# Kernel optimization log

Measured on AMD Instinct MI355X. Metric: run time of the kernel, lower is better.

The kernel has to match this reference:

```python
import jax, jax.numpy as jnp
import numpy as np

B, T_SRC, T_TGT = 2048, 32, 32
D = 512            # d_model
D_SRC, D_TGT = 100, 80
L = 2              # n_layers


def setup_inputs() -> dict:
    key = jax.random.key(0)
    ks = jax.random.split(key, 16)
    s = 1.0 / float(np.sqrt(D))  # torch LSTM init scale
    u = lambda k, shape: jax.random.uniform(k, shape, jnp.float32, -s, s)
    return {
        "src": jax.random.randint(ks[0], (B, T_SRC), 0, D_SRC, dtype=jnp.int32),
        "tgt": jax.random.randint(ks[1], (B, T_TGT), 0, D_TGT, dtype=jnp.int32),
        "enc_emb": jax.random.normal(ks[2], (D_SRC, D), jnp.float32),
        "dec_emb": jax.random.normal(ks[3], (D_TGT, D), jnp.float32),
        "enc_Wih": u(ks[4], (L, 4 * D, D)),
        "enc_Whh": u(ks[5], (L, 4 * D, D)),
        "enc_bih": u(ks[6], (L, 4 * D)),
        "enc_bhh": u(ks[7], (L, 4 * D)),
        "dec_Wih": u(ks[8], (L, 4 * D, D)),
        "dec_Whh": u(ks[9], (L, 4 * D, D)),
        "dec_bih": u(ks[10], (L, 4 * D)),
        "dec_bhh": u(ks[11], (L, 4 * D)),
        "post_W": u(ks[12], (D_TGT, D)),
        "post_b": u(ks[13], (D_TGT,)),
    }


def lstm_cell(x, h, c, Wih, Whh, bih, bhh):
    # PyTorch gate order: i, f, g, o
    gates = x @ Wih.T + bih + h @ Whh.T + bhh  # [B, 4D]
    i, f, g, o = jnp.split(gates, 4, axis=-1)
    c_new = jax.nn.sigmoid(f) * c + jax.nn.sigmoid(i) * jnp.tanh(g)
    h_new = jax.nn.sigmoid(o) * jnp.tanh(c_new)
    return h_new, c_new


def reference(src, tgt, enc_emb, dec_emb, enc_Wih, enc_Whh, enc_bih, enc_bhh,
              dec_Wih, dec_Whh, dec_bih, dec_bhh, post_W, post_b):
    # Eval-mode forward: dropout = identity, teacher forcing disabled
    # (tf = random() < ratio AND self.training is False at inference).
    n_layers = enc_Wih.shape[0]
    Bb = src.shape[0]
    Dm = enc_emb.shape[1]

    # ---- encoder: multi-layer LSTM over src embeddings ----
    x = enc_emb[src].swapaxes(0, 1)  # [T_src, B, D]
    hs, cs = [], []
    z = jnp.zeros((Bb, Dm), x.dtype)
    for l in range(n_layers):
        def step(carry, xt, l=l):
            h, c = carry
            h, c = lstm_cell(xt, h, c, enc_Wih[l], enc_Whh[l], enc_bih[l], enc_bhh[l])
            return (h, c), h
        (hT, cT), x = jax.lax.scan(step, (z, z), x)
        hs.append(hT)
        cs.append(cT)
    h0 = jnp.stack(hs)  # [L, B, D]
    c0 = jnp.stack(cs)  # [L, B, D]

    prev0 = dec_emb[tgt[:, 0]]  # [B, D]

    def dec_step(carry, _):
        h, c, prev = carry
        x = prev
        new_h, new_c = [], []
        for l in range(n_layers):
            hl, cl = lstm_cell(x, h[l], c[l], dec_Wih[l], dec_Whh[l], dec_bih[l], dec_bhh[l])
            new_h.append(hl)
            new_c.append(cl)
            x = hl
        logits = x @ post_W.T + post_b          # [B, d_tgt]
        pred = jnp.argmax(logits, axis=-1)       # [B]
        prev = dec_emb[pred]                     # [B, D]
        return (jnp.stack(new_h), jnp.stack(new_c), prev), logits

    _, out = jax.lax.scan(dec_step, (h0, c0, prev0), None, length=tgt.shape[1])
    return out.swapaxes(0, 1)  # [B, T_tgt, d_tgt]
```

## Files before the change

kernel.cpp:

```cpp
#include <hip/hip_runtime.h>
#include <hip/hip_bf16.h>

#define B_  2048
#define T_  32
#define D_  512
#define G_  2048
#define VT_ 80
#define BD  (B_ * D_)
#define LWE ((size_t)G_ * D_)

typedef _Float16 half8 __attribute__((ext_vector_type(8)));
typedef _Float16 half4_t __attribute__((ext_vector_type(4)));
typedef float    f32x4 __attribute__((ext_vector_type(4)));

static __device__ __forceinline__ float sigm(float x) {
    return 1.0f / (1.0f + expf(-x));
}

typedef __attribute__((address_space(1))) unsigned int gas_u32;
typedef __attribute__((address_space(3))) unsigned int las_u32;
static __device__ __forceinline__ void glds16(const void* src, void* dst) {
    __builtin_amdgcn_global_load_lds(
        (gas_u32*)(unsigned long long)(size_t)src,
        (las_u32*)(unsigned int)(size_t)dst, 16, 0, 0);
}

#define WBX() do {                                        \
    asm volatile("s_waitcnt vmcnt(10)" ::: "memory");     \
    __builtin_amdgcn_s_barrier();                         \
    __builtin_amdgcn_sched_barrier(0);                    \
} while (0)

__global__ void zero_ws(int4* __restrict__ p, int n) {
    int i = blockIdx.x * blockDim.x + threadIdx.x;
    if (i < n) p[i] = int4{0, 0, 0, 0};
}
__global__ void init_pred(const int* __restrict__ tgt, int* __restrict__ pred) {
    int i = blockIdx.x * blockDim.x + threadIdx.x;
    if (i < B_) pred[i] = tgt[i * T_];
}

__global__ void split_weights(const float* __restrict__ s0, const float* __restrict__ s1,
                              const float* __restrict__ s2, const float* __restrict__ s3,
                              const float* __restrict__ s4, const float* __restrict__ s5,
                              _Float16* __restrict__ Wbase) {
    int g = blockIdx.x * blockDim.x + threadIdx.x;
    int mat = g >> 17;
    int rem = g & 131071;
    int np  = rem >> 6;
    int kq  = rem & 63;
    const float* src = (mat == 0) ? s0 : (mat == 1) ? s1 : (mat == 2) ? s2
                     : (mat == 3) ? s3 : (mat == 4) ? s4 : s5;
    int n = (np & 3) * D_ + (np >> 2);
    const float* sp = src + (size_t)n * D_ + kq * 8;
    float4 v0 = ((const float4*)sp)[0], v1 = ((const float4*)sp)[1];
    float x[8] = {v0.x, v0.y, v0.z, v0.w, v1.x, v1.y, v1.z, v1.w};
    _Float16 hi[8], lo[8];
    #pragma unroll
    for (int u = 0; u < 8; ++u) {
        hi[u] = (_Float16)x[u];
        lo[u] = (_Float16)(x[u] - (float)hi[u]);
    }
    int tile = (np >> 4) * 16 + (kq >> 2);
    int lane = (np & 15) | ((kq & 3) << 4);
    size_t e = (size_t)tile * 512 + (size_t)lane * 8;
    _Float16* Whi = Wbase + (size_t)mat * (2 * LWE);
    _Float16* Wlo = Whi + LWE;
    *(half8*)(Whi + e) = *(half8*)hi;
    *(half8*)(Wlo + e) = *(half8*)lo;
}

__global__ void split_postW(const float* __restrict__ pw,
                            _Float16* __restrict__ Ph, _Float16* __restrict__ Pl) {
    int g = blockIdx.x * blockDim.x + threadIdx.x;
    if (g >= VT_ * 64) return;
    int v = g >> 6, kq = g & 63;
    const float* sp = pw + (size_t)v * D_ + kq * 8;
    float4 v0 = ((const float4*)sp)[0], v1 = ((const float4*)sp)[1];
    float x[8] = {v0.x, v0.y, v0.z, v0.w, v1.x, v1.y, v1.z, v1.w};
    _Float16 hi[8], lo[8];
    #pragma unroll
    for (int u = 0; u < 8; ++u) {
        hi[u] = (_Float16)x[u];
        lo[u] = (_Float16)(x[u] - (float)hi[u]);
    }
    int tile = (v >> 4) * 16 + (kq >> 2);
    int lane = (v & 15) | ((kq & 3) << 4);
    size_t e = (size_t)tile * 512 + (size_t)lane * 8;
    *(half8*)(Ph + e) = *(half8*)hi;
    *(half8*)(Pl + e) = *(half8*)lo;
}

__global__ void perm_bias(const float* __restrict__ ebih, const float* __restrict__ ebhh,
                          const float* __restrict__ dbih, const float* __restrict__ dbhh,
                          float* __restrict__ biasP) {
    int i = blockIdx.x * blockDim.x + threadIdx.x;
    int cfg = i >> 11, np = i & 2047;
    int n = (np & 3) * D_ + (np >> 2);
    const float* bi = ((cfg < 2) ? ebih : dbih) + (cfg & 1) * G_;
    const float* bh = ((cfg < 2) ? ebhh : dbhh) + (cfg & 1) * G_;
    biasP[cfg * G_ + np] = bi[n] + bh[n];
}

__global__ __launch_bounds__(256) void compute_P(
    const float* __restrict__ enc_emb, const float* __restrict__ dec_emb,
    const float* __restrict__ encW0,   const float* __restrict__ decW0,
    float* __restrict__ P) {
    __shared__ float es[10][D_];
    __shared__ float part[4][64][10];
    int by = blockIdx.y;
    bool enc = (by < 10);
    int r0 = enc ? by * 10 : 100 + (by - 10) * 10;
    int s0 = enc ? by * 10 : (by - 10) * 10;
    const float* emb = enc ? enc_emb : dec_emb;
    const float* W   = enc ? encW0 : decW0;
    int tid = threadIdx.x;
    #pragma unroll
    for (int it = 0; it < 5; ++it) {
        int i4 = it * 256 + tid;
        int rr = i4 >> 7, cc = i4 & 127;
        ((float4*)es[rr])[cc] = ((const float4*)(emb + (size_t)(s0 + rr) * D_))[cc];
    }
    __syncthreads();
    int o   = tid & 63;
    int seg = tid >> 6;
    int np = blockIdx.x * 64 + o;
    int n = (np & 3) * D_ + (np >> 2);
    const float* wr = W + (size_t)n * D_ + seg * 128;
    float acc[10];
    #pragma unroll
    for (int rr = 0; rr < 10; ++rr) acc[rr] = 0.f;
    for (int k = 0; k < 128; k += 4) {
        float4 w4 = *(const float4*)(wr + k);
        int kb = seg * 128 + k;
        #pragma unroll
        for (int rr = 0; rr < 10; ++rr)
            acc[rr] += es[rr][kb] * w4.x + es[rr][kb+1] * w4.y
                     + es[rr][kb+2] * w4.z + es[rr][kb+3] * w4.w;
    }
    #pragma unroll
    for (int rr = 0; rr < 10; ++rr) part[seg][o][rr] = acc[rr];
    __syncthreads();
    for (int i = tid; i < 640; i += 256) {
        int o2 = i & 63, rr = i >> 6;
        P[(size_t)(r0 + rr) * G_ + blockIdx.x * 64 + o2] =
            (part[0][o2][rr] + part[1][o2][rr]) + (part[2][o2][rr] + part[3][o2][rr]);
    }
}

struct CellJob {
    const _Float16 *a0h, *a0l, *w0h, *w0l;
    int kclo0, kchi0;
    const _Float16 *a1h, *a1l, *w1h, *w1l;
    int kclo1, kchi1;
    const float *biasP;
    const float *P;
    const int  *idx;
    int idx_stride, emb_rows;
    float *c_io;
    _Float16 *hh_out, *hl_out;
};

__global__ __launch_bounds__(512, 2) void lstm_cell_mfma(CellJob J0, CellJob J1) {
    const CellJob J = (blockIdx.z == 0) ? J0 : J1;
    __shared__ __align__(128) char smem[65536];
    float (*gf)[68] = (float (*)[68])smem;

    const int tid  = threadIdx.x;
    const int w    = tid >> 6;
    const int lane = tid & 63;
    const int g    = w >> 2;
    const int mw   = w & 3;
    const int id   = blockIdx.x;
    const int xcd  = id & 7;
    const int rest = id >> 3;
    const int mt   = ((rest & 3) << 1) | (xcd >> 2);
    const int bx   = ((rest >> 2) << 2) | (xcd & 3);
    const int m0   = mt * 256;

    const _Float16* Ah = g ? J.a1h : J.a0h;
    const _Float16* Al = g ? J.a1l : J.a0l;
    const _Float16* Wh = g ? J.w1h : J.w0h;
    const _Float16* Wl = g ? J.w1l : J.w0l;
    const int kclo = g ? J.kclo1 : J.kclo0;
    const int kchi = g ? J.kchi1 : J.kchi0;

    const int afr = (m0 >> 4) + mw * 4;
    const int wfr = bx * 4;

    f32x4 acc[4][4];
    #pragma unroll
    for (int i = 0; i < 4; ++i)
        #pragma unroll
        for (int j = 0; j < 4; ++j) acc[i][j] = f32x4{0.f, 0.f, 0.f, 0.f};

    char* const sb = smem + w * 2048;
    const char* const rg0 = smem + (g << 13);

    auto stage = [&](int buf, int kc) {
        size_t toff = (((size_t)(wfr + (w & 3)) * 16 + kc) << 9) + (size_t)lane * 8;
        char* d = sb + buf * 16384;
        glds16(Wh + toff, d);
        glds16(Wl + toff, d + 1024);
    };
    auto ldA = [&](half8* A8, int kc) {
        size_t lo8 = (size_t)lane * 8;
        #pragma unroll
        for (int i = 0; i < 4; ++i) {
            size_t off = (((size_t)(afr + i) * 16 + kc) << 9) + lo8;
            A8[i]     = *(const half8*)(Ah + off);
            A8[4 + i] = *(const half8*)(Al + off);
        }
    };
    auto domfma = [&](const half8* A8, int buf) {
        const char* r = rg0 + buf * 16384;
        size_t lo16 = (size_t)lane * 16;
        #pragma unroll
        for (int j = 0; j < 4; ++j) {
            half8 Bh = *(const half8*)(r + j * 2048 + lo16);
            half8 Bl = *(const half8*)(r + j * 2048 + 1024 + lo16);
            #pragma unroll
            for (int i = 0; i < 4; ++i) {
                acc[i][j] = __builtin_amdgcn_mfma_f32_16x16x32_f16(A8[i], Bh, acc[i][j], 0, 0, 0);
                acc[i][j] = __builtin_amdgcn_mfma_f32_16x16x32_f16(A8[i], Bl, acc[i][j], 0, 0, 0);
                acc[i][j] = __builtin_amdgcn_mfma_f32_16x16x32_f16(A8[4 + i], Bh, acc[i][j], 0, 0, 0);
            }
        }
    };

    half8 A0[8], A1[8];
    const int nit = (kchi - kclo) >> 2;

    ldA(A0, kclo);
    stage(0, kclo);
    stage(1, kclo + 1);
    asm volatile("s_waitcnt vmcnt(0)" ::: "memory");
    __builtin_amdgcn_s_barrier();
    __builtin_amdgcn_sched_barrier(0);

    for (int it = 0; it < nit; ++it) {
        const int k0 = kclo + (it << 2);
        ldA(A1, k0 + 1); stage(2, k0 + 2); domfma(A0, 0); WBX();
        ldA(A0, k0 + 2); stage(3, k0 + 3); domfma(A1, 1); WBX();
        ldA(A1, k0 + 3); stage(0, k0 + 4); domfma(A0, 2); WBX();
        ldA(A0, k0 + 4); stage(1, k0 + 5); domfma(A1, 3); WBX();
    }
    asm volatile("s_waitcnt vmcnt(0)" ::: "memory");
    __syncthreads();

    const int rbase = (lane >> 4) << 2;
    const int cbase = lane & 15;
    for (int p = 0; p < 2; ++p) {
        if (g == 0 && (mw >> 1) == p) {
            #pragma unroll
            for (int i = 0; i < 4; ++i) {
                int mrow = (mw & 1) * 64 + i * 16 + rbase;
                #pragma unroll
                for (int j = 0; j < 4; ++j) {
                    int nc = j * 16 + cbase;
                    #pragma unroll
                    for (int r = 0; r < 4; ++r)
                        gf[mrow + r][nc] = acc[i][j][r];
                }
            }
        }
        __syncthreads();
        if (g == 1 && (mw >> 1) == p) {
            #pragma unroll
            for (int i = 0; i < 4; ++i) {
                int mrow = (mw & 1) * 64 + i * 16 + rbase;
                #pragma unroll
                for (int j = 0; j < 4; ++j) {
                    int nc = j * 16 + cbase;
                    #pragma unroll
                    for (int r = 0; r < 4; ++r)
                        gf[mrow + r][nc] += acc[i][j][r];
                }
            }
        }
        __syncthreads();
        {
            int mr = tid >> 2, q = tid & 3;
            int mg = m0 + p * 128 + mr;
            const float4* brow = (const float4*)(J.biasP + (bx << 6));
            const float4* Pr = nullptr;
            if (J.P) {
                int s = J.idx[mg * J.idx_stride];
                s = min(max(s, 0), J.emb_rows - 1);
                Pr = (const float4*)(J.P + (size_t)s * G_ + (bx << 6));
            }
            float* crow = J.c_io + (size_t)mg * D_ + (bx << 4) + (q << 2);
            float4 cv = *(float4*)crow;
            _Float16 hh4[4], hl4[4];
            #pragma unroll
            for (int e = 0; e < 4; ++e) {
                int dl = (q << 2) + e;
                float4 g4 = *(float4*)&gf[mr][dl << 2];
                float4 b4 = brow[dl];
                float gi = g4.x + b4.x, gF = g4.y + b4.y;
                float gg = g4.z + b4.z, go = g4.w + b4.w;
                if (Pr) {
                    float4 p4 = Pr[dl];
                    gi += p4.x; gF += p4.y; gg += p4.z; go += p4.w;
                }
                float cc = (&cv.x)[e];
                float cn = sigm(gF) * cc + sigm(gi) * tanhf(gg);
                float hn = sigm(go) * tanhf(cn);
                (&cv.x)[e] = cn;
                _Float16 hH = (_Float16)hn;
                hh4[e] = hH;
                hl4[e] = (_Float16)(hn - (float)hH);
            }
            *(float4*)crow = cv;
            int kk = (bx << 4) + (q << 2);
            size_t hoff = ((size_t)((mg >> 4) * 16 + (kk >> 5)) << 9)
                        + (size_t)((mg & 15) | (((kk >> 3) & 3) << 4)) * 8
                        + ((q & 1) << 2);
            *(half4_t*)(J.hh_out + hoff) = *(half4_t*)hh4;
            *(half4_t*)(J.hl_out + hoff) = *(half4_t*)hl4;
        }
        __syncthreads();
    }
}

__global__ __launch_bounds__(64) void logits_mfma(
    const _Float16* __restrict__ Ah, const _Float16* __restrict__ Al,
    const _Float16* __restrict__ Bh, const _Float16* __restrict__ Bl,
    const float* __restrict__ postb, float* __restrict__ out,
    int t, int* __restrict__ pred) {
    __shared__ float gf2[16][85];
    __shared__ float pb[VT_];
    const int lane = threadIdx.x;
    const int m0  = blockIdx.x * 16;
    const int afr = blockIdx.x;

    f32x4 acc[5];
    #pragma unroll
    for (int j = 0; j < 5; ++j) acc[j] = f32x4{0.f, 0.f, 0.f, 0.f};

    size_t lo8 = (size_t)lane * 8;
    for (int kc = 0; kc < 16; ++kc) {
        half8 Ahh, All, Bh8[5], Bl8[5];
        {
            size_t off = (((size_t)afr * 16 + kc) << 9) + lo8;
            Ahh = *(const half8*)(Ah + off);
            All = *(const half8*)(Al + off);
        }
        #pragma unroll
        for (int j = 0; j < 5; ++j) {
            size_t off = (((size_t)(j * 16 + kc)) << 9) + lo8;
            Bh8[j] = *(const half8*)(Bh + off);
            Bl8[j] = *(const half8*)(Bl + off);
        }
        #pragma unroll
        for (int j = 0; j < 5; ++j) {
            acc[j] = __builtin_amdgcn_mfma_f32_16x16x32_f16(Ahh, Bh8[j], acc[j], 0, 0, 0);
            acc[j] = __builtin_amdgcn_mfma_f32_16x16x32_f16(Ahh, Bl8[j], acc[j], 0, 0, 0);
            acc[j] = __builtin_amdgcn_mfma_f32_16x16x32_f16(All, Bh8[j], acc[j], 0, 0, 0);
        }
    }

    if (lane < 40) ((float2*)pb)[lane] = ((const float2*)postb)[lane];
    const int quad = lane >> 4, c = lane & 15;
    #pragma unroll
    for (int j = 0; j < 5; ++j)
        #pragma unroll
        for (int r = 0; r < 4; ++r)
            gf2[quad * 4 + r][j * 16 + c] = acc[j][r];
    __syncthreads();
    if (lane < 16) {
        int r = lane;
        float best = -3.4e38f; int bi = 0;
        #pragma unroll
        for (int v = 0; v < VT_; ++v) {
            float x = gf2[r][v] + pb[v];
            if (x > best) { best = x; bi = v; }
        }
        pred[m0 + r] = bi;
        float* orow = out + (size_t)(m0 + r) * (T_ * VT_) + (size_t)t * VT_;
        #pragma unroll
        for (int v4 = 0; v4 < VT_ / 4; ++v4) {
            float4 g4 = *(float4*)&gf2[r][v4 * 4];
            float4 b4 = *(float4*)&pb[v4 * 4];
            float4 o4 = {g4.x + b4.x, g4.y + b4.y, g4.z + b4.z, g4.w + b4.w};
            *(float4*)(orow + v4 * 4) = o4;
        }
    }
}

extern "C" void kernel_launch(void* const* d_in, const int* in_sizes, int n_in,
                              void* d_out, int out_size, void* d_ws, size_t ws_size,
                              hipStream_t stream) {
    (void)in_sizes; (void)n_in; (void)out_size; (void)ws_size;

    const int*   src     = (const int*)d_in[0];
    const int*   tgt     = (const int*)d_in[1];
    const float* enc_emb = (const float*)d_in[2];
    const float* dec_emb = (const float*)d_in[3];
    const float* enc_Wih = (const float*)d_in[4];
    const float* enc_Whh = (const float*)d_in[5];
    const float* enc_bih = (const float*)d_in[6];
    const float* enc_bhh = (const float*)d_in[7];
    const float* dec_Wih = (const float*)d_in[8];
    const float* dec_Whh = (const float*)d_in[9];
    const float* dec_bih = (const float*)d_in[10];
    const float* dec_bhh = (const float*)d_in[11];
    const float* post_W  = (const float*)d_in[12];
    const float* post_b  = (const float*)d_in[13];

    char* wsb = (char*)d_ws;
    int*   pred  = (int*)wsb;
    float* biasB = (float*)(wsb + 16384);
    float* Ptab  = (float*)(wsb + 16384 + 32768);
    char*  zbase = wsb + 16384 + 32768 + 180 * G_ * 4;
    float* C0 = (float*)zbase;
    float* C1 = C0 + BD;
    _Float16* Hh00 = (_Float16*)(C1 + BD);
    _Float16* Hh10 = Hh00 + BD;
    _Float16* Hl00 = Hh10 + BD;
    _Float16* Hl10 = Hl00 + BD;
    _Float16* Hh01 = Hl10 + BD;
    _Float16* Hh11 = Hh01 + BD;
    _Float16* Hl01 = Hh11 + BD;
    _Float16* Hl11 = Hl01 + BD;
    _Float16* Wb   = Hl11 + BD;
    _Float16* PwH  = Wb + 6 * 2 * LWE;
    _Float16* PwL  = PwH + (size_t)VT_ * D_;

    _Float16* Hhi[2][2] = { { Hh00, Hh01 }, { Hh10, Hh11 } };
    _Float16* Hlo[2][2] = { { Hl00, Hl01 }, { Hl10, Hl11 } };
    float*    Cp[2]     = { C0, C1 };
    auto WP = [&](int m, int pl) { return Wb + (size_t)m * (2 * LWE) + (size_t)pl * LWE; };

    float* out = (float*)d_out;

    zero_ws<<<4096, 256, 0, stream>>>((int4*)zbase, (16 * 1024 * 1024) / 16);
    init_pred<<<8, 256, 0, stream>>>(tgt, pred);
    split_weights<<<3072, 256, 0, stream>>>(
        enc_Whh, enc_Wih + LWE, enc_Whh + LWE,
        dec_Whh, dec_Wih + LWE, dec_Whh + LWE, Wb);
    split_postW<<<20, 256, 0, stream>>>(post_W, PwH, PwL);
    perm_bias<<<32, 256, 0, stream>>>(enc_bih, enc_bhh, dec_bih, dec_bhh, biasB);
    {
        dim3 gP(32, 18);
        compute_P<<<gP, 256, 0, stream>>>(enc_emb, dec_emb, enc_Wih, dec_Wih, Ptab);
    }

    dim3 grid1(256, 1, 1);
    dim3 grid2(256, 1, 2);
    int c0 = 0, c1 = 0;

    auto mkL0 = [&](bool enc, const int* ix, int stride, int rows) {
        int m = enc ? 0 : 3;
        CellJob j;
        j.a0h = Hhi[0][c0]; j.a0l = Hlo[0][c0];
        j.w0h = WP(m, 0);   j.w0l = WP(m, 1);
        j.kclo0 = 0; j.kchi0 = 8;
        j.a1h = Hhi[0][c0]; j.a1l = Hlo[0][c0];
        j.w1h = WP(m, 0);   j.w1l = WP(m, 1);
        j.kclo1 = 8; j.kchi1 = 16;
        j.biasP = biasB + (enc ? 0 : 2) * G_;
        j.P = enc ? Ptab : Ptab + (size_t)100 * G_;
        j.idx = ix; j.idx_stride = stride; j.emb_rows = rows;
        j.c_io = Cp[0];
        j.hh_out = Hhi[0][c0 ^ 1]; j.hl_out = Hlo[0][c0 ^ 1];
        return j;
    };
    auto mkL1 = [&](bool enc) {
        int mi = enc ? 1 : 4, mh = enc ? 2 : 5;
        CellJob j;
        j.a0h = Hhi[0][c0]; j.a0l = Hlo[0][c0];
        j.w0h = WP(mi, 0);  j.w0l = WP(mi, 1);
        j.kclo0 = 0; j.kchi0 = 16;
        j.a1h = Hhi[1][c1]; j.a1l = Hlo[1][c1];
        j.w1h = WP(mh, 0);  j.w1l = WP(mh, 1);
        j.kclo1 = 0; j.kchi1 = 16;
        j.biasP = biasB + (enc ? 1 : 3) * G_;
        j.P = nullptr; j.idx = nullptr; j.idx_stride = 0; j.emb_rows = 0;
        j.c_io = Cp[1];
        j.hh_out = Hhi[1][c1 ^ 1]; j.hl_out = Hlo[1][c1 ^ 1];
        return j;
    };

    {
        CellJob j0 = mkL0(true, src + 0, T_, 100);
        lstm_cell_mfma<<<grid1, 512, 0, stream>>>(j0, j0);
        c0 ^= 1;
        for (int t = 0; t < T_ - 1; ++t) {
            CellJob jA = mkL1(true);
            CellJob jB = mkL0(true, src + t + 1, T_, 100);
            lstm_cell_mfma<<<grid2, 512, 0, stream>>>(jA, jB);
            c1 ^= 1; c0 ^= 1;
        }
        CellJob jZ = mkL1(true);
        lstm_cell_mfma<<<grid1, 512, 0, stream>>>(jZ, jZ);
        c1 ^= 1;
    }

    for (int t = 0; t < T_; ++t) {
        CellJob j0 = mkL0(false, pred, 1, VT_);
        lstm_cell_mfma<<<grid1, 512, 0, stream>>>(j0, j0);
        c0 ^= 1;
        CellJob j1 = mkL1(false);
        lstm_cell_mfma<<<grid1, 512, 0, stream>>>(j1, j1);
        c1 ^= 1;
        logits_mfma<<<128, 64, 0, stream>>>(
            Hhi[1][c1], Hlo[1][c1], PwH, PwL, post_b, out, t, pred);
    }
}
```

Baseline: 4.603 ms.

## Stage activations in LDS and stream weights through registers in LSTM cell GEMM

The LSTM cell GEMM now stages the activation tile (A, hi/lo fp16 split) into LDS with global_load_lds and loads weight fragments directly into registers, swapping the previous roles. Each wave now covers 128 rows by 32 columns instead of 64 by 64. Shared memory grows to 128 KB of dynamic LDS with a double buffer per K-group, and the gate epilogue runs in a single pass of 8 elements per thread instead of two passes. The larger LDS footprint likely limits occupancy to one block per CU despite launch_bounds(512,2), and the deeper pipeline is simplified to two buffers with full barriers.

```diff
diff --git a/kernel.cpp b/kernel.cpp
--- a/kernel.cpp
+++ b/kernel.cpp
@@ -13,6 +13,8 @@
 typedef _Float16 half4_t __attribute__((ext_vector_type(4)));
 typedef float    f32x4 __attribute__((ext_vector_type(4)));
 
+#define MFMA16(a, b, c) __builtin_amdgcn_mfma_f32_16x16x32_f16(a, b, c, 0, 0, 0)
+
 static __device__ __forceinline__ float sigm(float x) {
     return 1.0f / (1.0f + expf(-x));
 }
@@ -24,12 +26,6 @@
         (gas_u32*)(unsigned long long)(size_t)src,
         (las_u32*)(unsigned int)(size_t)dst, 16, 0, 0);
 }
-
-#define WBX() do {                                        \
-    asm volatile("s_waitcnt vmcnt(10)" ::: "memory");     \
-    __builtin_amdgcn_s_barrier();                         \
-    __builtin_amdgcn_sched_barrier(0);                    \
-} while (0)
 
 __global__ void zero_ws(int4* __restrict__ p, int n) {
     int i = blockIdx.x * blockDim.x + threadIdx.x;
@@ -161,16 +157,19 @@
     _Float16 *hh_out, *hl_out;
 };
 
-__global__ __launch_bounds__(512, 2) void lstm_cell_mfma(CellJob J0, CellJob J1) {
+__global__ void __launch_bounds__(512, 2) lstm_cell_mfma(CellJob J0, CellJob J1) {
+    extern __shared__ char smem[];
+    float (*gf)[68] = (float (*)[68])smem;
+
     const CellJob J = (blockIdx.z == 0) ? J0 : J1;
-    __shared__ __align__(128) char smem[65536];
-    float (*gf)[68] = (float (*)[68])smem;
 
     const int tid  = threadIdx.x;
     const int w    = tid >> 6;
     const int lane = tid & 63;
     const int g    = w >> 2;
-    const int mw   = w & 3;
+    const int v    = w & 3;
+    const int mw   = v >> 1;
+    const int nw   = v & 1;
     const int id   = blockIdx.x;
     const int xcd  = id & 7;
     const int rest = id >> 3;
@@ -185,141 +184,148 @@
     const int kclo = g ? J.kclo1 : J.kclo0;
     const int kchi = g ? J.kchi1 : J.kchi0;
 
-    const int afr = (m0 >> 4) + mw * 4;
-    const int wfr = bx * 4;
-
-    f32x4 acc[4][4];
-    #pragma unroll
-    for (int i = 0; i < 4; ++i)
-        #pragma unroll
-        for (int j = 0; j < 4; ++j) acc[i][j] = f32x4{0.f, 0.f, 0.f, 0.f};
-
-    char* const sb = smem + w * 2048;
-    const char* const rg0 = smem + (g << 13);
-
-    auto stage = [&](int buf, int kc) {
-        size_t toff = (((size_t)(wfr + (w & 3)) * 16 + kc) << 9) + (size_t)lane * 8;
-        char* d = sb + buf * 16384;
-        glds16(Wh + toff, d);
-        glds16(Wl + toff, d + 1024);
+    const int wfr = bx * 4 + nw * 2;
+
+    f32x4 acc[8][2];
+    #pragma unroll
+    for (int f = 0; f < 8; ++f) {
+        acc[f][0] = f32x4{0.f, 0.f, 0.f, 0.f};
+        acc[f][1] = f32x4{0.f, 0.f, 0.f, 0.f};
+    }
+
+    char* const gbase = smem + (g << 16);
+
+    auto stageA = [&](int buf, int kc) {
+        char* d = gbase + buf * 32768 + (v << 13);
+        #pragma unroll
+        for (int s = 0; s < 8; ++s) {
+            const int t    = v * 8 + s;
+            const int fIdx = t >> 1;
+            const _Float16* sp = ((t & 1) ? Al : Ah)
+                + (((size_t)((m0 >> 4) + fIdx) * 16 + kc) << 9) + (size_t)lane * 8;
+            glds16(sp, d + s * 1024);
+        }
     };
-    auto ldA = [&](half8* A8, int kc) {
-        size_t lo8 = (size_t)lane * 8;
-        #pragma unroll
-        for (int i = 0; i < 4; ++i) {
-            size_t off = (((size_t)(afr + i) * 16 + kc) << 9) + lo8;
-            A8[i]     = *(const half8*)(Ah + off);
-            A8[4 + i] = *(const half8*)(Al + off);
+    auto ldB = [&](half8* Bv, int kc) {
+        #pragma unroll
+        for (int jj = 0; jj < 2; ++jj) {
+            size_t off = (((size_t)(wfr + jj) * 16 + kc) << 9) + (size_t)lane * 8;
+            Bv[jj * 2]     = *(const half8*)(Wh + off);
+            Bv[jj * 2 + 1] = *(const half8*)(Wl + off);
         }
     };
-    auto domfma = [&](const half8* A8, int buf) {
-        const char* r = rg0 + buf * 16384;
-        size_t lo16 = (size_t)lane * 16;
-        #pragma unroll
-        for (int j = 0; j < 4; ++j) {
-            half8 Bh = *(const half8*)(r + j * 2048 + lo16);
-            half8 Bl = *(const half8*)(r + j * 2048 + 1024 + lo16);
+    auto compute = [&](const half8* Bv, int buf) {
+        const char* r = gbase + buf * 32768 + (mw << 14) + lane * 16;
+        half8 Ar[16];
+        #pragma unroll
+        for (int t = 0; t < 16; ++t)
+            Ar[t] = *(const half8*)(r + t * 1024);
+        #pragma unroll
+        for (int jj = 0; jj < 2; ++jj) {
             #pragma unroll
-            for (int i = 0; i < 4; ++i) {
-                acc[i][j] = __builtin_amdgcn_mfma_f32_16x16x32_f16(A8[i], Bh, acc[i][j], 0, 0, 0);
-                acc[i][j] = __builtin_amdgcn_mfma_f32_16x16x32_f16(A8[i], Bl, acc[i][j], 0, 0, 0);
-                acc[i][j] = __builtin_amdgcn_mfma_f32_16x16x32_f16(A8[4 + i], Bh, acc[i][j], 0, 0, 0);
+            for (int f = 0; f < 8; ++f) {
+                acc[f][jj] = MFMA16(Ar[2*f],     Bv[jj*2],     acc[f][jj]);
+                acc[f][jj] = MFMA16(Ar[2*f],     Bv[jj*2 + 1], acc[f][jj]);
+                acc[f][jj] = MFMA16(Ar[2*f + 1], Bv[jj*2],     acc[f][jj]);
             }
         }
     };
 
-    half8 A0[8], A1[8];
-    const int nit = (kchi - kclo) >> 2;
-
-    ldA(A0, kclo);
-    stage(0, kclo);
-    stage(1, kclo + 1);
-    asm volatile("s_waitcnt vmcnt(0)" ::: "memory");
-    __builtin_amdgcn_s_barrier();
-    __builtin_amdgcn_sched_barrier(0);
-
-    for (int it = 0; it < nit; ++it) {
-        const int k0 = kclo + (it << 2);
-        ldA(A1, k0 + 1); stage(2, k0 + 2); domfma(A0, 0); WBX();
-        ldA(A0, k0 + 2); stage(3, k0 + 3); domfma(A1, 1); WBX();
-        ldA(A1, k0 + 3); stage(0, k0 + 4); domfma(A0, 2); WBX();
-        ldA(A0, k0 + 4); stage(1, k0 + 5); domfma(A1, 3); WBX();
-    }
-    asm volatile("s_waitcnt vmcnt(0)" ::: "memory");
+    half8 B0[4], B1[4];
+    const int P = kchi - kclo;
+
+    stageA(0, kclo);
+    ldB(B0, kclo);
     __syncthreads();
+
+    for (int u = 0; u < P; u += 2) {
+        {
+            const int kc = kclo + u;
+            stageA(1, kc + 1);
+            ldB(B1, kc + 1);
+            __builtin_amdgcn_sched_barrier(0);
+            compute(B0, 0);
+            __syncthreads();
+        }
+        {
+            const int kc = kclo + u + 1;
+            if (u + 2 < P) {
+                stageA(0, kc + 1);
+                ldB(B0, kc + 1);
+            }
+            __builtin_amdgcn_sched_barrier(0);
+            compute(B1, 1);
+            __syncthreads();
+        }
+    }
 
     const int rbase = (lane >> 4) << 2;
     const int cbase = lane & 15;
-    for (int p = 0; p < 2; ++p) {
-        if (g == 0 && (mw >> 1) == p) {
+    if (g == 0) {
+        #pragma unroll
+        for (int f = 0; f < 8; ++f)
             #pragma unroll
-            for (int i = 0; i < 4; ++i) {
-                int mrow = (mw & 1) * 64 + i * 16 + rbase;
+            for (int jj = 0; jj < 2; ++jj) {
+                int nc = nw * 32 + jj * 16 + cbase;
                 #pragma unroll
-                for (int j = 0; j < 4; ++j) {
-                    int nc = j * 16 + cbase;
-                    #pragma unroll
-                    for (int r = 0; r < 4; ++r)
-                        gf[mrow + r][nc] = acc[i][j][r];
-                }
+                for (int r = 0; r < 4; ++r)
+                    gf[mw * 128 + f * 16 + rbase + r][nc] = acc[f][jj][r];
             }
-        }
-        __syncthreads();
-        if (g == 1 && (mw >> 1) == p) {
+    }
+    __syncthreads();
+    if (g == 1) {
+        #pragma unroll
+        for (int f = 0; f < 8; ++f)
             #pragma unroll
-            for (int i = 0; i < 4; ++i) {
-                int mrow = (mw & 1) * 64 + i * 16 + rbase;
+            for (int jj = 0; jj < 2; ++jj) {
+                int nc = nw * 32 + jj * 16 + cbase;
                 #pragma unroll
-                for (int j = 0; j < 4; ++j) {
-                    int nc = j * 16 + cbase;
-                    #pragma unroll
-                    for (int r = 0; r < 4; ++r)
-                        gf[mrow + r][nc] += acc[i][j][r];
-                }
+                for (int r = 0; r < 4; ++r)
+                    gf[mw * 128 + f * 16 + rbase + r][nc] += acc[f][jj][r];
             }
-        }
-        __syncthreads();
-        {
-            int mr = tid >> 2, q = tid & 3;
-            int mg = m0 + p * 128 + mr;
-            const float4* brow = (const float4*)(J.biasP + (bx << 6));
-            const float4* Pr = nullptr;
-            if (J.P) {
-                int s = J.idx[mg * J.idx_stride];
-                s = min(max(s, 0), J.emb_rows - 1);
-                Pr = (const float4*)(J.P + (size_t)s * G_ + (bx << 6));
+    }
+    __syncthreads();
+    {
+        const int mr = tid >> 1;
+        const int q  = tid & 1;
+        const int mg = m0 + mr;
+        const float4* brow = (const float4*)(J.biasP + (bx << 6));
+        const float4* Pr = nullptr;
+        if (J.P) {
+            int s = J.idx[mg * J.idx_stride];
+            s = min(max(s, 0), J.emb_rows - 1);
+            Pr = (const float4*)(J.P + (size_t)s * G_ + (bx << 6));
+        }
+        float* crow = J.c_io + (size_t)mg * D_ + (bx << 4) + (q << 3);
+        float4 cv0 = ((float4*)crow)[0];
+        float4 cv1 = ((float4*)crow)[1];
+        _Float16 hh8[8], hl8[8];
+        #pragma unroll
+        for (int e = 0; e < 8; ++e) {
+            const int dl = (q << 3) + e;
+            float4 g4 = *(float4*)&gf[mr][dl << 2];
+            float4 b4 = brow[dl];
+            float gi = g4.x + b4.x, gF = g4.y + b4.y;
+            float gg = g4.z + b4.z, go = g4.w + b4.w;
+            if (Pr) {
+                float4 p4 = Pr[dl];
+                gi += p4.x; gF += p4.y; gg += p4.z; go += p4.w;
             }
-            float* crow = J.c_io + (size_t)mg * D_ + (bx << 4) + (q << 2);
-            float4 cv = *(float4*)crow;
-            _Float16 hh4[4], hl4[4];
-            #pragma unroll
-            for (int e = 0; e < 4; ++e) {
-                int dl = (q << 2) + e;
-                float4 g4 = *(float4*)&gf[mr][dl << 2];
-                float4 b4 = brow[dl];
-                float gi = g4.x + b4.x, gF = g4.y + b4.y;
-                float gg = g4.z + b4.z, go = g4.w + b4.w;
-                if (Pr) {
-                    float4 p4 = Pr[dl];
-                    gi += p4.x; gF += p4.y; gg += p4.z; go += p4.w;
-                }
-                float cc = (&cv.x)[e];
-                float cn = sigm(gF) * cc + sigm(gi) * tanhf(gg);
-                float hn = sigm(go) * tanhf(cn);
-                (&cv.x)[e] = cn;
-                _Float16 hH = (_Float16)hn;
-                hh4[e] = hH;
-                hl4[e] = (_Float16)(hn - (float)hH);
-            }
-            *(float4*)crow = cv;
-            int kk = (bx << 4) + (q << 2);
-            size_t hoff = ((size_t)((mg >> 4) * 16 + (kk >> 5)) << 9)
-                        + (size_t)((mg & 15) | (((kk >> 3) & 3) << 4)) * 8
-                        + ((q & 1) << 2);
-            *(half4_t*)(J.hh_out + hoff) = *(half4_t*)hh4;
-            *(half4_t*)(J.hl_out + hoff) = *(half4_t*)hl4;
-        }
-        __syncthreads();
+            float cc = (e < 4) ? (&cv0.x)[e] : (&cv1.x)[e - 4];
+            float cn = sigm(gF) * cc + sigm(gi) * tanhf(gg);
+            float hn = sigm(go) * tanhf(cn);
+            if (e < 4) (&cv0.x)[e] = cn; else (&cv1.x)[e - 4] = cn;
+            _Float16 hH = (_Float16)hn;
+            hh8[e] = hH;
+            hl8[e] = (_Float16)(hn - (float)hH);
+        }
+        ((float4*)crow)[0] = cv0;
+        ((float4*)crow)[1] = cv1;
+        const int kk0 = (bx << 4) + (q << 3);
+        size_t hbase = ((size_t)((mg >> 4) * 16 + (kk0 >> 5)) << 9)
+                     + (size_t)((mg & 15) | (((kk0 >> 3) & 3) << 4)) * 8;
+        *(half8*)(J.hh_out + hbase) = *(half8*)hh8;
+        *(half8*)(J.hl_out + hbase) = *(half8*)hl8;
     }
 }
 
@@ -354,9 +360,9 @@
         }
         #pragma unroll
         for (int j = 0; j < 5; ++j) {
-            acc[j] = __builtin_amdgcn_mfma_f32_16x16x32_f16(Ahh, Bh8[j], acc[j], 0, 0, 0);
-            acc[j] = __builtin_amdgcn_mfma_f32_16x16x32_f16(Ahh, Bl8[j], acc[j], 0, 0, 0);
-            acc[j] = __builtin_amdgcn_mfma_f32_16x16x32_f16(All, Bh8[j], acc[j], 0, 0, 0);
+            acc[j] = MFMA16(Ahh, Bh8[j], acc[j]);
+            acc[j] = MFMA16(Ahh, Bl8[j], acc[j]);
+            acc[j] = MFMA16(All, Bh8[j], acc[j]);
         }
     }
 
@@ -444,6 +450,13 @@
     {
         dim3 gP(32, 18);
         compute_P<<<gP, 256, 0, stream>>>(enc_emb, dec_emb, enc_Wih, dec_Wih, Ptab);
+    }
+
+    static int s_attr = 0;
+    if (!s_attr) {
+        hipFuncSetAttribute((const void*)lstm_cell_mfma,
+                            hipFuncAttributeMaxDynamicSharedMemorySize, 131072);
+        s_attr = 1;
     }
 
     dim3 grid1(256, 1, 1);
@@ -484,25 +497,25 @@
 
     {
         CellJob j0 = mkL0(true, src + 0, T_, 100);
-        lstm_cell_mfma<<<grid1, 512, 0, stream>>>(j0, j0);
+        lstm_cell_mfma<<<grid1, 512, 131072, stream>>>(j0, j0);
         c0 ^= 1;
         for (int t = 0; t < T_ - 1; ++t) {
             CellJob jA = mkL1(true);
             CellJob jB = mkL0(true, src + t + 1, T_, 100);
-            lstm_cell_mfma<<<grid2, 512, 0, stream>>>(jA, jB);
+            lstm_cell_mfma<<<grid2, 512, 131072, stream>>>(jA, jB);
             c1 ^= 1; c0 ^= 1;
         }
         CellJob jZ = mkL1(true);
-        lstm_cell_mfma<<<grid1, 512, 0, stream>>>(jZ, jZ);
+        lstm_cell_mfma<<<grid1, 512, 131072, stream>>>(jZ, jZ);
         c1 ^= 1;
     }
 
     for (int t = 0; t < T_; ++t) {
         CellJob j0 = mkL0(false, pred, 1, VT_);
-        lstm_cell_mfma<<<grid1, 512, 0, stream>>>(j0, j0);
+        lstm_cell_mfma<<<grid1, 512, 131072, stream>>>(j0, j0);
         c0 ^= 1;
         CellJob j1 = mkL1(false);
-        lstm_cell_mfma<<<grid1, 512, 0, stream>>>(j1, j1);
+        lstm_cell_mfma<<<grid1, 512, 131072, stream>>>(j1, j1);
         c1 ^= 1;
         logits_mfma<<<128, 64, 0, stream>>>(
             Hhi[1][c1], Hlo[1][c1], PwH, PwL, post_b, out, t, pred);
```

Result: faster. 4.471 ms (-2.9%).
